# Kernel tuning notes

Measured on AMD Instinct MI355X. Metric: run time of the kernel, lower is better.

Reference implementation:

```python
import jax, jax.numpy as jnp
import numpy as np

N_ATOMS = 300000
D_IN = 256


def setup_inputs() -> dict:
    key = jax.random.key(0)
    ks = jax.random.split(key, 8)

    def xavier(k, fan_in, fan_out):
        limit = float(np.sqrt(6.0 / (fan_in + fan_out)))
        return jax.random.uniform(k, (fan_in, fan_out), jnp.float32, -limit, limit)

    density = jax.random.normal(ks[0], (N_ATOMS, D_IN), jnp.float32)
    species = jax.random.randint(ks[1], (N_ATOMS,), -1, 10, jnp.int64)
    return {
        "density": density,
        "species": species,
        "W1": xavier(ks[2], 256, 512), "b1": jnp.zeros((512,), jnp.float32),
        "W2": xavier(ks[3], 512, 512), "b2": jnp.zeros((512,), jnp.float32),
        "W3": xavier(ks[4], 512, 256), "b3": jnp.zeros((256,), jnp.float32),
        "W4": xavier(ks[5], 256, 1),   "b4": jnp.zeros((1,), jnp.float32),
    }


def reference(density, species, W1, b1, W2, b2, W3, b3, W4, b4):
    # Equivalent to torch's nonzero-gather -> MLP -> scatter into zeros:
    # compute the MLP on all rows, then zero rows where species <= -0.5.
    h = jax.nn.silu(density @ W1 + b1)   # [N, 512]
    h = jax.nn.silu(h @ W2 + b2)         # [N, 512]
    h = jax.nn.silu(h @ W3 + b3)         # [N, 256]
    out = h @ W4 + b4                    # [N, 1]
    mask = species > -0.5                # valid atoms
    return jnp.where(mask[:, None], out, jnp.zeros((), out.dtype))
```

## Files before the change

kernel.cpp:

```cpp
#include <hip/hip_runtime.h>

typedef _Float16 half8 __attribute__((ext_vector_type(8)));
typedef _Float16 half4 __attribute__((ext_vector_type(4)));
typedef float f32x4 __attribute__((ext_vector_type(4)));
typedef float f32x16 __attribute__((ext_vector_type(16)));

__global__ void prep_weights(const float* __restrict__ W1, const float* __restrict__ W2,
                             const float* __restrict__ W3, const float* __restrict__ W4,
                             _Float16* __restrict__ wt1, _Float16* __restrict__ wt2,
                             _Float16* __restrict__ wt3, _Float16* __restrict__ w4h) {
  int idx = blockIdx.x * blockDim.x + threadIdx.x;
  if (idx < 512 * 256) {
    int k = idx >> 9, n = idx & 511;
    int off = (((n >> 5) * 16 + (k >> 4)) << 9) + (n & 31) * 8 + (((k >> 3) & 1) << 8) + (k & 7);
    wt1[off] = (_Float16)W1[idx];
    return;
  }
  int i2 = idx - 512 * 256;
  if (i2 < 512 * 512) {
    int k = i2 >> 9, n = i2 & 511;
    int off = (((n >> 5) * 32 + (k >> 4)) << 9) + (n & 31) * 8 + (((k >> 3) & 1) << 8) + (k & 7);
    wt2[off] = (_Float16)W2[i2];
    return;
  }
  int i3 = i2 - 512 * 512;
  if (i3 < 512 * 256) {
    int k = i3 >> 8, n = i3 & 255;
    int off = (((n >> 5) * 32 + (k >> 4)) << 9) + (n & 31) * 8 + (((k >> 3) & 1) << 8) + (k & 7);
    wt3[off] = (_Float16)W3[i3];
    return;
  }
  int i4 = i3 - 512 * 256;
  if (i4 < 256) w4h[i4] = (_Float16)W4[i4];
}

__device__ __forceinline__ float fast_silu(float s) {
  float e = __expf(-s);
  float d = 1.0f + e;
  float r;
  asm("v_rcp_f32 %0, %1" : "=v"(r) : "v"(d));
  return s * r;
}


#define MFMA(a, b, c) __builtin_amdgcn_mfma_f32_32x32x16_f16(a, b, c, 0, 0, 0)

template <int FT, int AT, int KS, int PIN, int POUT>
__device__ __forceinline__ void layer(const _Float16* __restrict__ wt,
                                      const float* __restrict__ bias,
                                      char* __restrict__ Hb,
                                      int wfeat, int lane) {
  const int lr = lane & 31;
  const int lh = lane >> 5;
  const int n0 = wfeat * (FT * 32);
  const int s0 = (lr & 31) << 4;
  const char* Bp = Hb + lr * PIN;
  const char* wp = (const char*)wt + (size_t)(wfeat * FT * KS) * 1024 + lh * 512 + lr * 16;

  f32x16 acc[FT][AT];
#pragma unroll
  for (int f = 0; f < FT; ++f)
#pragma unroll
    for (int a = 0; a < AT; ++a) acc[f][a] = (f32x16)0.0f;

  half8 Af[FT], Ag[FT], Bf[AT], Bg[AT];
#pragma unroll
  for (int f = 0; f < FT; ++f) Af[f] = *(const half8*)(wp + f * (KS * 1024));
#pragma unroll
  for (int a = 0; a < AT; ++a)
    Bf[a] = *(const half8*)(Bp + a * 32 * PIN + ((lh * 16) ^ s0));

#pragma unroll 1
  for (int ks = 0; ks < KS - 2; ks += 2) {
#pragma unroll
    for (int f = 0; f < FT; ++f)
      Ag[f] = *(const half8*)(wp + f * (KS * 1024) + (ks + 1) * 1024);
#pragma unroll
    for (int a = 0; a < AT; ++a)
      Bg[a] = *(const half8*)(Bp + a * 32 * PIN + (((ks + 1) * 32 + lh * 16) ^ s0));
#pragma unroll
    for (int f = 0; f < FT; ++f)
#pragma unroll
      for (int a = 0; a < AT; ++a) acc[f][a] = MFMA(Af[f], Bf[a], acc[f][a]);
#pragma unroll
    for (int f = 0; f < FT; ++f)
      Af[f] = *(const half8*)(wp + f * (KS * 1024) + (ks + 2) * 1024);
#pragma unroll
    for (int a = 0; a < AT; ++a)
      Bf[a] = *(const half8*)(Bp + a * 32 * PIN + (((ks + 2) * 32 + lh * 16) ^ s0));
#pragma unroll
    for (int f = 0; f < FT; ++f)
#pragma unroll
      for (int a = 0; a < AT; ++a) acc[f][a] = MFMA(Ag[f], Bg[a], acc[f][a]);
  }
#pragma unroll
  for (int f = 0; f < FT; ++f)
    Ag[f] = *(const half8*)(wp + f * (KS * 1024) + (KS - 1) * 1024);
#pragma unroll
  for (int a = 0; a < AT; ++a)
    Bg[a] = *(const half8*)(Bp + a * 32 * PIN + ((((KS - 1) * 32) + lh * 16) ^ s0));
#pragma unroll
  for (int f = 0; f < FT; ++f)
#pragma unroll
    for (int a = 0; a < AT; ++a) acc[f][a] = MFMA(Af[f], Bf[a], acc[f][a]);
#pragma unroll
  for (int f = 0; f < FT; ++f)
#pragma unroll
    for (int a = 0; a < AT; ++a) acc[f][a] = MFMA(Ag[f], Bg[a], acc[f][a]);

  __syncthreads();

#pragma unroll
  for (int f = 0; f < FT; ++f) {
#pragma unroll
    for (int rg = 0; rg < 4; ++rg) {
      const int feat = n0 + f * 32 + rg * 8 + lh * 4;
      const f32x4 bv = *(const f32x4*)(bias + feat);
#pragma unroll
      for (int a = 0; a < AT; ++a) {
        half4 h;
#pragma unroll
        for (int r = 0; r < 4; ++r) h[r] = (_Float16)fast_silu(acc[f][a][rg * 4 + r] + bv[r]);
        const int row = a * 32 + lr;
        *(half4*)(Hb + row * POUT + ((feat * 2) ^ ((row & 31) << 4))) = h;
      }
    }
  }
}

extern "C" __global__ void __launch_bounds__(512, 4)
mlp_kernel(const float* __restrict__ X, const int* __restrict__ species,
           const _Float16* __restrict__ wt1, const float* __restrict__ b1,
           const _Float16* __restrict__ wt2, const float* __restrict__ b2,
           const _Float16* __restrict__ wt3, const float* __restrict__ b3,
           const _Float16* __restrict__ w4h, const float* __restrict__ b4,
           float* __restrict__ out, int natoms) {
  __shared__ __align__(16) char H[64 * 1024];
  const int tid = threadIdx.x;
  const int lane = tid & 63;
  const int wid = tid >> 6;
  const long abase = (long)blockIdx.x * 64;

  {
    const int r = tid >> 3, cg = tid & 7;
    long g = abase + r;
    const long gmax = (long)natoms - 1;
    if (g > gmax) g = gmax;
    const float* xp = X + g * 256;
    const int sw = (r & 31) << 4;
#pragma unroll
    for (int j = 0; j < 8; ++j) {
      const int colh = cg * 4 + j * 32;
      f32x4 v = *(const f32x4*)(xp + colh);
      half4 h;
#pragma unroll
      for (int e = 0; e < 4; ++e) h[e] = (_Float16)v[e];
      *(half4*)(H + r * 512 + ((colh * 2) ^ sw)) = h;
    }
  }
  __syncthreads();

  layer<2, 2, 16, 512, 1024>(wt1, b1, H, wid, lane);
  __syncthreads();
  layer<2, 2, 32, 1024, 1024>(wt2, b2, H, wid, lane);
  __syncthreads();
  layer<1, 2, 32, 1024, 1024>(wt3, b3, H, wid, lane);
  __syncthreads();

  const int atom = tid >> 3, part = tid & 7;
  const int sw = (atom & 31) << 4;
  const char* h3 = H + atom * 1024;
  const _Float16* w4p = w4h + part * 32;
  float sum = 0.0f;
#pragma unroll
  for (int j = 0; j < 4; ++j) {
    half8 h = *(const half8*)(h3 + ((part * 64 + j * 16) ^ sw));
    half8 w = *(const half8*)(w4p + j * 8);
#pragma unroll
    for (int e = 0; e < 8; ++e) sum += (float)h[e] * (float)w[e];
  }
  sum += __shfl_xor(sum, 1);
  sum += __shfl_xor(sum, 2);
  sum += __shfl_xor(sum, 4);
  if (part == 0) {
    const long g = abase + atom;
    if (g < natoms) {
      float r = sum + b4[0];
      out[g] = (species[g] >= 0) ? r : 0.0f;
    }
  }
}

extern "C" void kernel_launch(void* const* d_in, const int* in_sizes, int n_in,
                              void* d_out, int out_size, void* d_ws, size_t ws_size,
                              hipStream_t stream) {
  const float* X = (const float*)d_in[0];
  const int* species = (const int*)d_in[1];
  const float* W1 = (const float*)d_in[2];
  const float* b1 = (const float*)d_in[3];
  const float* W2 = (const float*)d_in[4];
  const float* b2 = (const float*)d_in[5];
  const float* W3 = (const float*)d_in[6];
  const float* b3 = (const float*)d_in[7];
  const float* W4 = (const float*)d_in[8];
  const float* b4 = (const float*)d_in[9];
  float* out = (float*)d_out;
  const int natoms = in_sizes[0] / 256;

  char* ws = (char*)d_ws;
  _Float16* wt1 = (_Float16*)(ws);
  _Float16* wt2 = (_Float16*)(ws + 262144);
  _Float16* wt3 = (_Float16*)(ws + 262144 + 524288);
  _Float16* w4h = (_Float16*)(ws + 262144 + 524288 + 262144);

  const int prep_total = 512 * 256 + 512 * 512 + 256 * 512 + 256;
  hipLaunchKernelGGL(prep_weights, dim3((prep_total + 255) / 256), dim3(256), 0, stream,
                     W1, W2, W3, W4, wt1, wt2, wt3, w4h);

  const int nblocks = (natoms + 63) / 64;
  hipLaunchKernelGGL(mlp_kernel, dim3(nblocks), dim3(512), 0, stream,
                     X, species, wt1, b1, wt2, b2, wt3, b3, w4h, b4, out, natoms);
}
```

Before: 394.1 us.

## Use persistent grid with staggered start, next-tile prefetch, and MFMA priority

Replaces one block per 64-atom tile with a persistent grid of at most 512 blocks that loop over tiles. Half the blocks sleep briefly at start so the co-resident blocks fall out of phase and one block's MFMA phase can overlap another's load and epilogue phases. It also touches the next tile's input rows to warm the cache, and raises wave priority around the MFMA bursts with s_setprio. The risks are lost time from the startup sleep, an extra barrier per tile, and load imbalance across the fixed grid.

Result: slower. 496.1 us (+25.9%).

```diff
diff --git a/kernel.cpp b/kernel.cpp
--- a/kernel.cpp
+++ b/kernel.cpp
@@ -78,20 +78,24 @@
 #pragma unroll
     for (int a = 0; a < AT; ++a)
       Bg[a] = *(const half8*)(Bp + a * 32 * PIN + (((ks + 1) * 32 + lh * 16) ^ s0));
+    __builtin_amdgcn_s_setprio(1);
 #pragma unroll
     for (int f = 0; f < FT; ++f)
 #pragma unroll
       for (int a = 0; a < AT; ++a) acc[f][a] = MFMA(Af[f], Bf[a], acc[f][a]);
+    __builtin_amdgcn_s_setprio(0);
 #pragma unroll
     for (int f = 0; f < FT; ++f)
       Af[f] = *(const half8*)(wp + f * (KS * 1024) + (ks + 2) * 1024);
 #pragma unroll
     for (int a = 0; a < AT; ++a)
       Bf[a] = *(const half8*)(Bp + a * 32 * PIN + (((ks + 2) * 32 + lh * 16) ^ s0));
+    __builtin_amdgcn_s_setprio(1);
 #pragma unroll
     for (int f = 0; f < FT; ++f)
 #pragma unroll
       for (int a = 0; a < AT; ++a) acc[f][a] = MFMA(Ag[f], Bg[a], acc[f][a]);
+    __builtin_amdgcn_s_setprio(0);
   }
 #pragma unroll
   for (int f = 0; f < FT; ++f)
@@ -99,6 +103,7 @@
 #pragma unroll
   for (int a = 0; a < AT; ++a)
     Bg[a] = *(const half8*)(Bp + a * 32 * PIN + ((((KS - 1) * 32) + lh * 16) ^ s0));
+  __builtin_amdgcn_s_setprio(1);
 #pragma unroll
   for (int f = 0; f < FT; ++f)
 #pragma unroll
@@ -107,6 +112,7 @@
   for (int f = 0; f < FT; ++f)
 #pragma unroll
     for (int a = 0; a < AT; ++a) acc[f][a] = MFMA(Ag[f], Bg[a], acc[f][a]);
+  __builtin_amdgcn_s_setprio(0);
 
   __syncthreads();
 
@@ -139,55 +145,78 @@
   const int tid = threadIdx.x;
   const int lane = tid & 63;
   const int wid = tid >> 6;
-  const long abase = (long)blockIdx.x * 64;
-
-  {
-    const int r = tid >> 3, cg = tid & 7;
-    long g = abase + r;
-    const long gmax = (long)natoms - 1;
-    if (g > gmax) g = gmax;
-    const float* xp = X + g * 256;
-    const int sw = (r & 31) << 4;
-#pragma unroll
-    for (int j = 0; j < 8; ++j) {
-      const int colh = cg * 4 + j * 32;
-      f32x4 v = *(const f32x4*)(xp + colh);
-      half4 h;
-#pragma unroll
-      for (int e = 0; e < 4; ++e) h[e] = (_Float16)v[e];
-      *(half4*)(H + r * 512 + ((colh * 2) ^ sw)) = h;
-    }
-  }
-  __syncthreads();
-
-  layer<2, 2, 16, 512, 1024>(wt1, b1, H, wid, lane);
-  __syncthreads();
-  layer<2, 2, 32, 1024, 1024>(wt2, b2, H, wid, lane);
-  __syncthreads();
-  layer<1, 2, 32, 1024, 1024>(wt3, b3, H, wid, lane);
-  __syncthreads();
-
-  const int atom = tid >> 3, part = tid & 7;
-  const int sw = (atom & 31) << 4;
-  const char* h3 = H + atom * 1024;
-  const _Float16* w4p = w4h + part * 32;
-  float sum = 0.0f;
-#pragma unroll
-  for (int j = 0; j < 4; ++j) {
-    half8 h = *(const half8*)(h3 + ((part * 64 + j * 16) ^ sw));
-    half8 w = *(const half8*)(w4p + j * 8);
-#pragma unroll
-    for (int e = 0; e < 8; ++e) sum += (float)h[e] * (float)w[e];
-  }
-  sum += __shfl_xor(sum, 1);
-  sum += __shfl_xor(sum, 2);
-  sum += __shfl_xor(sum, 4);
-  if (part == 0) {
-    const long g = abase + atom;
-    if (g < natoms) {
-      float r = sum + b4[0];
-      out[g] = (species[g] >= 0) ? r : 0.0f;
-    }
+  const int ntiles = (natoms + 63) >> 6;
+  const long gmax = (long)natoms - 1;
+
+  if (blockIdx.x >= (gridDim.x >> 1)) {
+#pragma unroll
+    for (int i = 0; i < 4; ++i) __builtin_amdgcn_s_sleep(127);
+  }
+
+  for (int t = blockIdx.x; t < ntiles; t += gridDim.x) {
+    const long abase = (long)t << 6;
+
+    {
+      const int r = tid >> 3, cg = tid & 7;
+      long g = abase + r;
+      if (g > gmax) g = gmax;
+      const float* xp = X + g * 256;
+      const int sw = (r & 31) << 4;
+#pragma unroll
+      for (int j = 0; j < 8; ++j) {
+        const int colh = cg * 4 + j * 32;
+        f32x4 v = *(const f32x4*)(xp + colh);
+        half4 h;
+#pragma unroll
+        for (int e = 0; e < 4; ++e) h[e] = (_Float16)v[e];
+        *(half4*)(H + r * 512 + ((colh * 2) ^ sw)) = h;
+      }
+    }
+    __syncthreads();
+
+    {
+      const long tn = (long)t + gridDim.x;
+      if ((tn << 6) < (long)natoms) {
+        long gp = (tn << 6) * 256 + tid * 32;
+        const long gmaxf = (long)natoms * 256 - 1;
+        if (gp > gmaxf) gp = gmaxf;
+        float v = X[gp];
+        asm volatile("" ::"v"(v));
+      }
+    }
+
+    layer<2, 2, 16, 512, 1024>(wt1, b1, H, wid, lane);
+    __syncthreads();
+    layer<2, 2, 32, 1024, 1024>(wt2, b2, H, wid, lane);
+    __syncthreads();
+    layer<1, 2, 32, 1024, 1024>(wt3, b3, H, wid, lane);
+    __syncthreads();
+
+    {
+      const int atom = tid >> 3, part = tid & 7;
+      const int sw = (atom & 31) << 4;
+      const char* h3 = H + atom * 1024;
+      const _Float16* w4p = w4h + part * 32;
+      float sum = 0.0f;
+#pragma unroll
+      for (int j = 0; j < 4; ++j) {
+        half8 h = *(const half8*)(h3 + ((part * 64 + j * 16) ^ sw));
+        half8 w = *(const half8*)(w4p + j * 8);
+#pragma unroll
+        for (int e = 0; e < 8; ++e) sum += (float)h[e] * (float)w[e];
+      }
+      sum += __shfl_xor(sum, 1);
+      sum += __shfl_xor(sum, 2);
+      sum += __shfl_xor(sum, 4);
+      if (part == 0) {
+        const long g = abase + atom;
+        if (g < natoms) {
+          float r = sum + b4[0];
+          out[g] = (species[g] >= 0) ? r : 0.0f;
+        }
+      }
+    }
+    __syncthreads();
   }
 }
 
@@ -217,7 +246,8 @@
   hipLaunchKernelGGL(prep_weights, dim3((prep_total + 255) / 256), dim3(256), 0, stream,
                      W1, W2, W3, W4, wt1, wt2, wt3, w4h);
 
-  const int nblocks = (natoms + 63) / 64;
+  const int ntiles = (natoms + 63) / 64;
+  const int nblocks = ntiles < 512 ? ntiles : 512;
   hipLaunchKernelGGL(mlp_kernel, dim3(nblocks), dim3(512), 0, stream,
                      X, species, wt1, b1, wt2, b2, wt3, b3, w4h, b4, out, natoms);
 }
```
